# Kernel tuning notes

Hardware: AMD Instinct MI355X
Metric: run time of the kernel (lower is better)

## Reference

```python
import jax, jax.numpy as jnp
import numpy as np

DIM = 3072
DIM_HEAD = 128
HEADS = 16
KV_DIM = 2048
INNER = DIM_HEAD * HEADS  # 2048


def layernorm(x, g, b, eps=1e-5):
    mu = jnp.mean(x, axis=-1, keepdims=True)
    var = jnp.mean((x - mu) ** 2, axis=-1, keepdims=True)
    return (x - mu) * jax.lax.rsqrt(var + eps) * g + b


def setup_inputs() -> dict:
    key = jax.random.key(0)
    ks = jax.random.split(key, 6)
    b, n1, n2 = 2, 4096, 1024
    x = jax.random.normal(ks[0], (b, n1, KV_DIM), dtype=jnp.float32)
    latents = jax.random.normal(ks[1], (b, n2, DIM), dtype=jnp.float32)
    # Linear weights stored [in, out] (torch stores [out, in]; math is x @ W)
    Wq = jax.random.normal(ks[2], (DIM, INNER), dtype=jnp.float32) * 0.02
    Wkv = jax.random.normal(ks[3], (KV_DIM, 2 * INNER), dtype=jnp.float32) * 0.02
    Wout = jax.random.normal(ks[4], (INNER, DIM), dtype=jnp.float32) * 0.02
    ln1_g = jnp.ones((KV_DIM,), jnp.float32)
    ln1_b = jnp.zeros((KV_DIM,), jnp.float32)
    ln2_g = jnp.ones((DIM,), jnp.float32)
    ln2_b = jnp.zeros((DIM,), jnp.float32)
    return {"x": x, "latents": latents, "ln1_g": ln1_g, "ln1_b": ln1_b,
            "ln2_g": ln2_g, "ln2_b": ln2_b, "Wq": Wq, "Wkv": Wkv, "Wout": Wout}


def reference(x, latents, ln1_g, ln1_b, ln2_g, ln2_b, Wq, Wkv, Wout):
    b, n2, _ = latents.shape
    xn = layernorm(x, ln1_g, ln1_b)          # (b, n1, kv_dim)
    ln = layernorm(latents, ln2_g, ln2_b)    # (b, n2, dim)
    q = ln @ Wq                               # (b, n2, inner)
    kv = xn @ Wkv                             # (b, n1, 2*inner)
    k, v = jnp.split(kv, 2, axis=-1)
    # (b, seq, h*d) -> (b, h, seq, d)
    def heads(t):
        bs, L, _ = t.shape
        return t.reshape(bs, L, HEADS, DIM_HEAD).transpose(0, 2, 1, 3)
    q, k, v = heads(q), heads(k), heads(v)
    scale = 1.0 / np.sqrt(np.sqrt(DIM_HEAD)).astype(np.float32)
    logits = jnp.einsum('bhqd,bhkd->bhqk', q * scale, k * scale)
    w = jax.nn.softmax(logits.astype(jnp.float32), axis=-1).astype(logits.dtype)
    out = jnp.einsum('bhqk,bhkd->bhqd', w, v)  # (b, h, n2, d)
    out = out.transpose(0, 2, 1, 3).reshape(b, n2, INNER)
    return out @ Wout
```

## Files before the change

kernel.cpp:

```cpp
#include <hip/hip_runtime.h>
#include <stdint.h>

typedef unsigned short u16;
typedef unsigned int u32;
typedef __attribute__((ext_vector_type(4))) float f32x4;
typedef __attribute__((ext_vector_type(8))) __bf16 bf16x8;

#define N1T 4096
#define N2T 1024
#define DIMT 3072
#define KVD 2048
#define INN 2048
#define NH 16
#define DH 128

__device__ __forceinline__ u16 f2bf(float f) {
  u32 u = __builtin_bit_cast(u32, f);
  u = (u + 0x7fffu + ((u >> 16) & 1u)) >> 16;
  return (u16)u;
}

typedef __attribute__((address_space(1))) void gvoid_t;
typedef __attribute__((address_space(3))) void lvoid_t;

__device__ __forceinline__ void gload16(const void* g, void* l) {
  __builtin_amdgcn_global_load_lds((gvoid_t*)g, (lvoid_t*)l, 16, 0, 0);
}

template<int NV>
__global__ __launch_bounds__(256) void ln_cast_kernel(
    const float* __restrict__ X, const float* __restrict__ G,
    const float* __restrict__ B, u16* __restrict__ out) {
  const int D = NV * 1024;
  const int t = threadIdx.x;
  const size_t row = blockIdx.x;
  const float4* xr = (const float4*)(X + row * D);
  float4 v[NV];
  float s = 0.f, ss = 0.f;
#pragma unroll
  for (int i = 0; i < NV; ++i) {
    v[i] = xr[i * 256 + t];
    s += v[i].x + v[i].y + v[i].z + v[i].w;
    ss += v[i].x * v[i].x + v[i].y * v[i].y + v[i].z * v[i].z + v[i].w * v[i].w;
  }
#pragma unroll
  for (int off = 32; off; off >>= 1) {
    s += __shfl_xor(s, off);
    ss += __shfl_xor(ss, off);
  }
  __shared__ float red[2][4];
  const int wave = t >> 6, lane = t & 63;
  if (lane == 0) { red[0][wave] = s; red[1][wave] = ss; }
  __syncthreads();
  s = red[0][0] + red[0][1] + red[0][2] + red[0][3];
  ss = red[1][0] + red[1][1] + red[1][2] + red[1][3];
  const float mu = s / D;
  const float rstd = rsqrtf(ss / D - mu * mu + 1e-5f);
  u16* orow = out + row * D;
#pragma unroll
  for (int i = 0; i < NV; ++i) {
    const int idx = (i * 256 + t) * 4;
    float4 g4 = *(const float4*)(G + idx);
    float4 b4 = *(const float4*)(B + idx);
    union { ushort4 v4; u16 h[4]; } pk;
    pk.h[0] = f2bf((v[i].x - mu) * rstd * g4.x + b4.x);
    pk.h[1] = f2bf((v[i].y - mu) * rstd * g4.y + b4.y);
    pk.h[2] = f2bf((v[i].z - mu) * rstd * g4.z + b4.z);
    pk.h[3] = f2bf((v[i].w - mu) * rstd * g4.w + b4.w);
    *(ushort4*)(orow + idx) = pk.v4;
  }
}

__global__ __launch_bounds__(256) void tcast_kernel(
    const float* __restrict__ W, u16* __restrict__ WT, int K, int N) {
  __shared__ __align__(16) u16 tile[64][72];
  const int t = threadIdx.x;
  const int k0 = blockIdx.x * 64, n0 = blockIdx.y * 64;
#pragma unroll
  for (int i = 0; i < 4; ++i) {
    int idx = i * 256 + t;
    int r = idx >> 4, c = (idx & 15) << 2;
    float4 v = *(const float4*)(W + (size_t)(k0 + r) * N + n0 + c);
    union { ushort4 v4; u16 h[4]; } pk;
    pk.h[0] = f2bf(v.x); pk.h[1] = f2bf(v.y);
    pk.h[2] = f2bf(v.z); pk.h[3] = f2bf(v.w);
    *(ushort4*)&tile[r][c] = pk.v4;
  }
  __syncthreads();
#pragma unroll
  for (int j = 0; j < 2; ++j) {
    int cid = j * 256 + t;
    int nr = cid >> 3, kc = (cid & 7) << 3;
    union { uint4 v4; u16 h[8]; } pk;
#pragma unroll
    for (int jj = 0; jj < 8; ++jj) pk.h[jj] = tile[kc + jj][nr];
    *(uint4*)(WT + (size_t)(n0 + nr) * K + k0 + kc) = pk.v4;
  }
}

template<int BF16OUT>
__global__ __launch_bounds__(256) void gemm_bt_kernel(
    const u16* __restrict__ A, size_t Az,
    const u16* __restrict__ Bt, size_t Btz,
    void* __restrict__ Cv, size_t Cz,
    int M, int N, int K, float scale) {
  __shared__ __align__(16) u16 As[128 * 64];
  __shared__ __align__(16) u16 Bs[128 * 64];
  A += (size_t)blockIdx.z * Az;
  Bt += (size_t)blockIdx.z * Btz;
  const int t = threadIdx.x, lane = t & 63, wave = t >> 6;
  const int m0 = blockIdx.x * 128, n0 = blockIdx.y * 128;
  const int wr = (wave >> 1) * 64, wc = (wave & 1) * 64;
  const int fr = lane & 15, fk = (lane >> 4) * 8;
  f32x4 acc[4][4];
#pragma unroll
  for (int i = 0; i < 4; ++i)
#pragma unroll
    for (int j = 0; j < 4; ++j)
#pragma unroll
      for (int r = 0; r < 4; ++r) acc[i][j][r] = 0.f;
  const int srow = t >> 3;
  const int scb = (t & 7) * 16;
  const int nk = K >> 6;
  for (int kt = 0; kt < nk; ++kt) {
    const char* Ab = (const char*)(A + (size_t)kt * 64);
    const char* Bb = (const char*)(Bt + (size_t)kt * 64);
#pragma unroll
    for (int r = 0; r < 4; ++r) {
      int row = srow + r * 32;
      gload16(Ab + (size_t)(m0 + row) * K * 2 + scb, (char*)As + t * 16 + r * 4096);
      gload16(Bb + (size_t)(n0 + row) * K * 2 + scb, (char*)Bs + t * 16 + r * 4096);
    }
    __syncthreads();
#pragma unroll
    for (int kk = 0; kk < 2; ++kk) {
      bf16x8 af[4], bfr[4];
#pragma unroll
      for (int i = 0; i < 4; ++i)
        af[i] = *(const bf16x8*)&As[(wr + i * 16 + fr) * 64 + kk * 32 + fk];
#pragma unroll
      for (int j = 0; j < 4; ++j)
        bfr[j] = *(const bf16x8*)&Bs[(wc + j * 16 + fr) * 64 + kk * 32 + fk];
#pragma unroll
      for (int i = 0; i < 4; ++i)
#pragma unroll
        for (int j = 0; j < 4; ++j)
          acc[i][j] = __builtin_amdgcn_mfma_f32_16x16x32_bf16(af[i], bfr[j], acc[i][j], 0, 0, 0);
    }
    __syncthreads();
  }
  const int cr = (lane >> 4) * 4, cc = lane & 15;
#pragma unroll
  for (int i = 0; i < 4; ++i)
#pragma unroll
    for (int j = 0; j < 4; ++j) {
      const int row = m0 + wr + i * 16 + cr;
      const int col = n0 + wc + j * 16 + cc;
      if (BF16OUT) {
        u16* C = (u16*)Cv + (size_t)blockIdx.z * Cz;
#pragma unroll
        for (int r = 0; r < 4; ++r) C[(size_t)(row + r) * N + col] = f2bf(acc[i][j][r] * scale);
      } else {
        float* C = (float*)Cv + (size_t)blockIdx.z * Cz;
#pragma unroll
        for (int r = 0; r < 4; ++r) C[(size_t)(row + r) * N + col] = acc[i][j][r];
      }
    }
}

__device__ __forceinline__ void stage_region(const u16* __restrict__ G, int ldk,
                                             int rowbase, int colbase,
                                             u16* lds, int t) {
  const int srow = t >> 2, sc = t & 3;
  const int swz = (srow >> 1) & 3;
#pragma unroll
  for (int r = 0; r < 2; ++r) {
    int row = r * 128 + srow;
    gload16(G + (size_t)(rowbase + row) * ldk + colbase + (sc ^ swz) * 8,
            (char*)lds + t * 16 + r * 8192);
  }
}

#define GPHASE(MSUB, KK, STAGE_STMT, RELOAD_B, VM0)                               \
  {                                                                               \
    STAGE_STMT;                                                                   \
    const u16* Aarr = (KK) ? A1s : A0s;                                           \
    _Pragma("unroll")                                                             \
    for (int fi = 0; fi < 4; ++fi) {                                              \
      int rowa = RM + (MSUB) * 64 + fi * 16 + fr;                                 \
      af[fi] = *(const bf16x8*)((const char*)Aarr + rowa * 64 +                   \
                                ((q ^ ((rowa >> 1) & 3)) * 16));                  \
    }                                                                             \
    if (RELOAD_B) {                                                               \
      const u16* Barr = (KK) ? B1s : B0s;                                         \
      _Pragma("unroll")                                                           \
      for (int j = 0; j < 4; ++j) {                                               \
        int rowb = RN + j * 16 + fr;                                              \
        bf[j] = *(const bf16x8*)((const char*)Barr + rowb * 64 +                  \
                                 ((q ^ ((rowb >> 1) & 3)) * 16));                 \
      }                                                                           \
    }                                                                             \
    if (VM0) { asm volatile("s_waitcnt vmcnt(0)" ::: "memory"); }                 \
    else     { asm volatile("s_waitcnt vmcnt(2)" ::: "memory"); }                 \
    __builtin_amdgcn_s_barrier();                                                 \
    asm volatile("s_waitcnt lgkmcnt(0)" ::: "memory");                            \
    __builtin_amdgcn_sched_barrier(0);                                            \
    __builtin_amdgcn_s_setprio(1);                                                \
    _Pragma("unroll")                                                             \
    for (int fi = 0; fi < 4; ++fi)                                                \
      _Pragma("unroll")                                                           \
      for (int j = 0; j < 4; ++j)                                                 \
        acc[(MSUB) * 4 + fi][j] = __builtin_amdgcn_mfma_f32_16x16x32_bf16(        \
            af[fi], bf[j], acc[(MSUB) * 4 + fi][j], 0, 0, 0);                     \
    __builtin_amdgcn_s_setprio(0);                                                \
    __builtin_amdgcn_s_barrier();                                                 \
  }

template<int BF16OUT>
__global__ __launch_bounds__(512) void gemm256_kernel(
    const u16* __restrict__ A, size_t Az,
    const u16* __restrict__ Bt, size_t Btz,
    void* __restrict__ Cv, size_t Cz,
    int M, int N, int K, float scale) {
  __shared__ __align__(16) u16 A0s[256 * 32];
  __shared__ __align__(16) u16 A1s[256 * 32];
  __shared__ __align__(16) u16 B0s[256 * 32];
  __shared__ __align__(16) u16 B1s[256 * 32];
  A += (size_t)blockIdx.z * Az;
  Bt += (size_t)blockIdx.z * Btz;
  const int t = threadIdx.x, lane = t & 63, wave = t >> 6;
  const int m0 = blockIdx.x * 256, n0 = blockIdx.y * 256;
  const int RM = (wave >> 2) * 128, RN = (wave & 3) * 64;
  const int fr = lane & 15, q = lane >> 4;
  f32x4 acc[8][4];
#pragma unroll
  for (int i = 0; i < 8; ++i)
#pragma unroll
    for (int j = 0; j < 4; ++j)
#pragma unroll
      for (int r = 0; r < 4; ++r) acc[i][j][r] = 0.f;

  stage_region(Bt, K, n0, 0, B0s, t);
  stage_region(A, K, m0, 0, A0s, t);
  stage_region(Bt, K, n0, 32, B1s, t);
  asm volatile("s_waitcnt vmcnt(0)" ::: "memory");
  __builtin_amdgcn_s_barrier();

  const int nk = K >> 6;
#pragma unroll 1
  for (int kt = 0; kt < nk; ++kt) {
    const bool last = (kt == nk - 1);
    bf16x8 af[4], bf[4];
    GPHASE(0, 0, stage_region(A, K, m0, kt * 64 + 32, A1s, t), true, false)
    GPHASE(1, 0, if (!last) stage_region(Bt, K, n0, (kt + 1) * 64, B0s, t), false, last)
    GPHASE(1, 1, if (!last) stage_region(A, K, m0, (kt + 1) * 64, A0s, t), true, last)
    GPHASE(0, 1, if (!last) stage_region(Bt, K, n0, (kt + 1) * 64 + 32, B1s, t), false, last)
  }

  const int cr = (lane >> 4) * 4, cc = lane & 15;
#pragma unroll
  for (int i = 0; i < 8; ++i)
#pragma unroll
    for (int j = 0; j < 4; ++j) {
      const int row = m0 + RM + i * 16 + cr;
      const int col = n0 + RN + j * 16 + cc;
      if (BF16OUT) {
        u16* C = (u16*)Cv + (size_t)blockIdx.z * Cz;
#pragma unroll
        for (int r = 0; r < 4; ++r) C[(size_t)(row + r) * N + col] = f2bf(acc[i][j][r] * scale);
      } else {
        float* C = (float*)Cv + (size_t)blockIdx.z * Cz;
#pragma unroll
        for (int r = 0; r < 4; ++r) C[(size_t)(row + r) * N + col] = acc[i][j][r];
      }
    }
}

__device__ __forceinline__ void stage_kv(const u16* Kbase, const u16* Vbase,
                                         int kv0, char* ks, char* vs, int t) {
  const int ks_row = t >> 4, ks_cb = (t & 15) * 16;
  const int vs_row = t >> 3, vs_cb = (t & 7) * 16;
#pragma unroll
  for (int r = 0; r < 2; ++r) {
    int row = ks_row + r * 32;
    int srccb = ks_cb ^ ((row & 15) << 4);
    gload16((const char*)(Kbase + (size_t)(kv0 + row) * INN) + srccb, ks + t * 16 + r * 8192);
  }
#pragma unroll
  for (int r = 0; r < 2; ++r) {
    int row = vs_row + r * 64;
    int srccb = vs_cb ^ ((row & 7) << 4);
    gload16((const char*)(Vbase + (size_t)row * N1T + kv0) + srccb, vs + t * 16 + r * 8192);
  }
}

__global__ __launch_bounds__(512) void attn_kernel(
    const u16* __restrict__ Q, const u16* __restrict__ Kb,
    const u16* __restrict__ Vt, u16* __restrict__ O) {
  __shared__ __align__(16) u16 Ks[2][64 * 128];
  __shared__ __align__(16) u16 Vs[2][128 * 64];
  __shared__ __align__(16) u16 Ps[8][16][72];
  const int t = threadIdx.x, lane = t & 63, wave = t >> 6;
  const int bid = blockIdx.x;
  const int xcd = bid & 7, idx = bid >> 3;
  const int bh = (xcd << 2) | (idx >> 3);
  const int q0 = (idx & 7) * 128;
  const int b = bh >> 4, h = bh & 15;
  const int fr = lane & 15, fk = (lane >> 4) * 8;
  const int quad16 = (lane >> 4) * 16;

  bf16x8 qf[4];
  {
    const u16* qrow = Q + (size_t)(b * N2T + q0 + wave * 16 + fr) * INN + h * DH;
#pragma unroll
    for (int c = 0; c < 4; ++c) qf[c] = *(const bf16x8*)(qrow + c * 32 + fk);
  }
  bf16x8 ones;
#pragma unroll
  for (int j = 0; j < 8; ++j) ones[j] = (__bf16)1.0f;

  float m_run[4], l_run[4];
  f32x4 o_acc[8];
#pragma unroll
  for (int r = 0; r < 4; ++r) { m_run[r] = -1e30f; l_run[r] = 0.f; }
#pragma unroll
  for (int i = 0; i < 8; ++i)
#pragma unroll
    for (int r = 0; r < 4; ++r) o_acc[i][r] = 0.f;

  const u16* Kbase = Kb + (size_t)(b * N1T) * INN + h * DH;
  const u16* Vbase = Vt + ((size_t)b * INN + h * DH) * N1T;

  const int NT = N1T / 64;
  int cur = 0;
  stage_kv(Kbase, Vbase, 0, (char*)&Ks[0][0], (char*)&Vs[0][0], t);
  for (int tile = 0; tile < NT; ++tile) {
    if (tile + 1 < NT) {
      stage_kv(Kbase, Vbase, (tile + 1) * 64, (char*)&Ks[cur ^ 1][0],
               (char*)&Vs[cur ^ 1][0], t);
      asm volatile("s_waitcnt vmcnt(4)" ::: "memory");
    } else {
      asm volatile("s_waitcnt vmcnt(0)" ::: "memory");
    }
    __builtin_amdgcn_s_barrier();
    __builtin_amdgcn_sched_barrier(0);
    const char* KsC = (const char*)&Ks[cur][0];
    const char* VsC = (const char*)&Vs[cur][0];

    f32x4 s[4];
#pragma unroll
    for (int ni = 0; ni < 4; ++ni) {
#pragma unroll
      for (int r = 0; r < 4; ++r) s[ni][r] = 0.f;
#pragma unroll
      for (int c = 0; c < 4; ++c) {
        int row = ni * 16 + fr;
        int byteoff = row * 256 + ((c * 64 + quad16) ^ ((row & 15) << 4));
        bf16x8 kf = *(const bf16x8*)(KsC + byteoff);
        s[ni] = __builtin_amdgcn_mfma_f32_16x16x32_bf16(qf[c], kf, s[ni], 0, 0, 0);
      }
    }
    float pmax[4];
#pragma unroll
    for (int r = 0; r < 4; ++r) {
      float mt = fmaxf(fmaxf(s[0][r], s[1][r]), fmaxf(s[2][r], s[3][r]));
#pragma unroll
      for (int d = 1; d < 16; d <<= 1) mt = fmaxf(mt, __shfl_xor(mt, d));
      pmax[r] = mt;
    }
    bool ok = (pmax[0] <= m_run[0] + 8.f) & (pmax[1] <= m_run[1] + 8.f) &
              (pmax[2] <= m_run[2] + 8.f) & (pmax[3] <= m_run[3] + 8.f);
    if (!__all(ok)) {
#pragma unroll
      for (int r = 0; r < 4; ++r) {
        float mnew = fmaxf(m_run[r], pmax[r]);
        float alpha = __expf(m_run[r] - mnew);
        m_run[r] = mnew;
        l_run[r] *= alpha;
#pragma unroll
        for (int ni2 = 0; ni2 < 8; ++ni2) o_acc[ni2][r] *= alpha;
      }
    }
#pragma unroll
    for (int r = 0; r < 4; ++r)
#pragma unroll
      for (int ni = 0; ni < 4; ++ni) s[ni][r] = __expf(s[ni][r] - m_run[r]);
#pragma unroll
    for (int ni = 0; ni < 4; ++ni)
#pragma unroll
      for (int r = 0; r < 4; ++r)
        Ps[wave][(lane >> 4) * 4 + r][fr + ni * 16] = f2bf(s[ni][r]);
    asm volatile("s_waitcnt lgkmcnt(0)" ::: "memory");
    __builtin_amdgcn_sched_barrier(0);
    bf16x8 pa[2];
#pragma unroll
    for (int c2 = 0; c2 < 2; ++c2) pa[c2] = *(const bf16x8*)&Ps[wave][fr][c2 * 32 + fk];
    f32x4 lt;
#pragma unroll
    for (int r = 0; r < 4; ++r) lt[r] = 0.f;
    lt = __builtin_amdgcn_mfma_f32_16x16x32_bf16(pa[0], ones, lt, 0, 0, 0);
    lt = __builtin_amdgcn_mfma_f32_16x16x32_bf16(pa[1], ones, lt, 0, 0, 0);
#pragma unroll
    for (int r = 0; r < 4; ++r) l_run[r] += lt[r];
#pragma unroll
    for (int ni2 = 0; ni2 < 8; ++ni2) {
#pragma unroll
      for (int c2 = 0; c2 < 2; ++c2) {
        int row = ni2 * 16 + fr;
        int byteoff = row * 128 + ((c2 * 64 + quad16) ^ ((row & 7) << 4));
        bf16x8 vf = *(const bf16x8*)(VsC + byteoff);
        o_acc[ni2] = __builtin_amdgcn_mfma_f32_16x16x32_bf16(pa[c2], vf, o_acc[ni2], 0, 0, 0);
      }
    }
    __builtin_amdgcn_sched_barrier(0);
    __builtin_amdgcn_s_barrier();
    cur ^= 1;
  }
  const int cr = (lane >> 4) * 4;
  u16* orow = O + (size_t)(b * N2T + q0 + wave * 16) * INN + h * DH;
#pragma unroll
  for (int r = 0; r < 4; ++r) {
    float inv = 1.0f / l_run[r];
#pragma unroll
    for (int ni2 = 0; ni2 < 8; ++ni2)
      orow[(size_t)(cr + r) * INN + ni2 * 16 + fr] = f2bf(o_acc[ni2][r] * inv);
  }
}

extern "C" void kernel_launch(void* const* d_in, const int* in_sizes, int n_in,
                              void* d_out, int out_size, void* d_ws, size_t ws_size,
                              hipStream_t stream) {
  const float* x = (const float*)d_in[0];
  const float* latents = (const float*)d_in[1];
  const float* ln1g = (const float*)d_in[2];
  const float* ln1b = (const float*)d_in[3];
  const float* ln2g = (const float*)d_in[4];
  const float* ln2b = (const float*)d_in[5];
  const float* Wq = (const float*)d_in[6];
  const float* Wkv = (const float*)d_in[7];
  const float* Wout = (const float*)d_in[8];

  char* w = (char*)d_ws;
  u16* xn = (u16*)w;   w += (size_t)8192 * 2048 * 2;
  u16* lnb = (u16*)w;  w += (size_t)2048 * 3072 * 2;
  u16* WqT = (u16*)w;  w += (size_t)2048 * 3072 * 2;
  u16* WkvT = (u16*)w; w += (size_t)4096 * 2048 * 2;
  u16* WoT = (u16*)w;  w += (size_t)3072 * 2048 * 2;
  u16* qb = (u16*)w;   w += (size_t)2048 * 2048 * 2;
  u16* kb = (u16*)w;   w += (size_t)8192 * 2048 * 2;
  u16* vtb = (u16*)w;  w += (size_t)2 * 2048 * 4096 * 2;
  u16* ab = (u16*)w;   w += (size_t)2048 * 2048 * 2;

  dim3 blk(256);
  tcast_kernel<<<dim3(48, 32), blk, 0, stream>>>(Wq, WqT, 3072, 2048);
  tcast_kernel<<<dim3(32, 64), blk, 0, stream>>>(Wkv, WkvT, 2048, 4096);
  tcast_kernel<<<dim3(32, 48), blk, 0, stream>>>(Wout, WoT, 2048, 3072);
  ln_cast_kernel<2><<<8192, blk, 0, stream>>>(x, ln1g, ln1b, xn);
  ln_cast_kernel<3><<<2048, blk, 0, stream>>>(latents, ln2g, ln2b, lnb);

  const float scale = 0.29730177875068026f;
  gemm_bt_kernel<1><<<dim3(16, 16, 1), blk, 0, stream>>>(
      lnb, 0, WqT, 0, qb, 0, 2048, 2048, 3072, scale);
  gemm256_kernel<1><<<dim3(32, 8, 1), dim3(512), 0, stream>>>(
      xn, 0, WkvT, 0, kb, 0, 8192, 2048, 2048, scale);
  gemm256_kernel<1><<<dim3(8, 16, 2), dim3(512), 0, stream>>>(
      WkvT + (size_t)2048 * 2048, 0, xn, (size_t)4096 * 2048,
      vtb, (size_t)2048 * 4096, 2048, 4096, 2048, 1.0f);
  attn_kernel<<<dim3(256), dim3(512), 0, stream>>>(qb, kb, vtb, ab);
  gemm_bt_kernel<0><<<dim3(16, 24, 1), blk, 0, stream>>>(
      ab, 0, WoT, 0, d_out, 0, 2048, 3072, 2048, 1.0f);
}
```

Baseline: 445.7 us.

## Transpose attention MFMA to keep P in registers and double KV tile

Reworks the flash-attention inner loop so that S^T = K·Q^T is computed, with keys along rows. Each lane then holds the probabilities for one query column and can pack them straight into bf16 MFMA operands with v_cvt_pk_bf16_f32. This removes the LDS round-trip for P, the ones-matrix MFMA used for row sums, and the per-row shuffle reductions. The KV tile grows from 64 to 128 keys with a new swizzle, halving the barrier count per sequence at the cost of more LDS. Outputs are written as 4-wide vector stores, and a key permutation (frp) keeps K and P orderings consistent.

```diff
diff --git a/kernel.cpp b/kernel.cpp
--- a/kernel.cpp
+++ b/kernel.cpp
@@ -18,6 +18,12 @@
   u32 u = __builtin_bit_cast(u32, f);
   u = (u + 0x7fffu + ((u >> 16) & 1u)) >> 16;
   return (u16)u;
+}
+
+__device__ __forceinline__ u32 cvtpk(float lo, float hi) {
+  u32 r;
+  asm volatile("v_cvt_pk_bf16_f32 %0, %1, %2" : "=v"(r) : "v"(lo), "v"(hi));
+  return r;
 }
 
 typedef __attribute__((address_space(1))) void gvoid_t;
@@ -276,38 +282,42 @@
     }
 }
 
+#define KVB 128
+__device__ __forceinline__ int swz4(int row) {
+  return ((row & 15) ^ (((row >> 4) & 1) << 2)) << 4;
+}
+
 __device__ __forceinline__ void stage_kv(const u16* Kbase, const u16* Vbase,
                                          int kv0, char* ks, char* vs, int t) {
-  const int ks_row = t >> 4, ks_cb = (t & 15) * 16;
-  const int vs_row = t >> 3, vs_cb = (t & 7) * 16;
-#pragma unroll
-  for (int r = 0; r < 2; ++r) {
-    int row = ks_row + r * 32;
-    int srccb = ks_cb ^ ((row & 15) << 4);
-    gload16((const char*)(Kbase + (size_t)(kv0 + row) * INN) + srccb, ks + t * 16 + r * 8192);
-  }
-#pragma unroll
-  for (int r = 0; r < 2; ++r) {
-    int row = vs_row + r * 64;
-    int srccb = vs_cb ^ ((row & 7) << 4);
-    gload16((const char*)(Vbase + (size_t)row * N1T + kv0) + srccb, vs + t * 16 + r * 8192);
+  const int col = (t & 15) * 16;
+#pragma unroll
+  for (int r = 0; r < 4; ++r) {
+    int row = (t >> 4) + r * 32;
+    gload16((const char*)(Kbase + (size_t)(kv0 + row) * INN) + (col ^ swz4(row)),
+            ks + t * 16 + r * 8192);
+  }
+#pragma unroll
+  for (int r = 0; r < 4; ++r) {
+    int row = (t >> 4) + r * 32;
+    gload16((const char*)(Vbase + (size_t)row * N1T + kv0) + (col ^ swz4(row)),
+            vs + t * 16 + r * 8192);
   }
 }
 
 __global__ __launch_bounds__(512) void attn_kernel(
     const u16* __restrict__ Q, const u16* __restrict__ Kb,
     const u16* __restrict__ Vt, u16* __restrict__ O) {
-  __shared__ __align__(16) u16 Ks[2][64 * 128];
-  __shared__ __align__(16) u16 Vs[2][128 * 64];
-  __shared__ __align__(16) u16 Ps[8][16][72];
+  __shared__ __align__(16) u16 Ks[2][KVB * 128];
+  __shared__ __align__(16) u16 Vs[2][128 * KVB];
   const int t = threadIdx.x, lane = t & 63, wave = t >> 6;
   const int bid = blockIdx.x;
   const int xcd = bid & 7, idx = bid >> 3;
   const int bh = (xcd << 2) | (idx >> 3);
   const int q0 = (idx & 7) * 128;
   const int b = bh >> 4, h = bh & 15;
-  const int fr = lane & 15, fk = (lane >> 4) * 8;
-  const int quad16 = (lane >> 4) * 16;
+  const int fr = lane & 15, quad = lane >> 4;
+  const int fk = quad * 8;
+  const int frp = fr + (fr & 12);
 
   bf16x8 qf[4];
   {
@@ -315,30 +325,25 @@
 #pragma unroll
     for (int c = 0; c < 4; ++c) qf[c] = *(const bf16x8*)(qrow + c * 32 + fk);
   }
-  bf16x8 ones;
-#pragma unroll
-  for (int j = 0; j < 8; ++j) ones[j] = (__bf16)1.0f;
-
-  float m_run[4], l_run[4];
-  f32x4 o_acc[8];
-#pragma unroll
-  for (int r = 0; r < 4; ++r) { m_run[r] = -1e30f; l_run[r] = 0.f; }
+
+  float m_run = -1e30f, l_run = 0.f;
+  f32x4 oT[8];
 #pragma unroll
   for (int i = 0; i < 8; ++i)
 #pragma unroll
-    for (int r = 0; r < 4; ++r) o_acc[i][r] = 0.f;
+    for (int r = 0; r < 4; ++r) oT[i][r] = 0.f;
 
   const u16* Kbase = Kb + (size_t)(b * N1T) * INN + h * DH;
   const u16* Vbase = Vt + ((size_t)b * INN + h * DH) * N1T;
 
-  const int NT = N1T / 64;
+  const int NT = N1T / KVB;
   int cur = 0;
   stage_kv(Kbase, Vbase, 0, (char*)&Ks[0][0], (char*)&Vs[0][0], t);
   for (int tile = 0; tile < NT; ++tile) {
     if (tile + 1 < NT) {
-      stage_kv(Kbase, Vbase, (tile + 1) * 64, (char*)&Ks[cur ^ 1][0],
+      stage_kv(Kbase, Vbase, (tile + 1) * KVB, (char*)&Ks[cur ^ 1][0],
                (char*)&Vs[cur ^ 1][0], t);
-      asm volatile("s_waitcnt vmcnt(4)" ::: "memory");
+      asm volatile("s_waitcnt vmcnt(8)" ::: "memory");
     } else {
       asm volatile("s_waitcnt vmcnt(0)" ::: "memory");
     }
@@ -347,83 +352,77 @@
     const char* KsC = (const char*)&Ks[cur][0];
     const char* VsC = (const char*)&Vs[cur][0];
 
-    f32x4 s[4];
-#pragma unroll
-    for (int ni = 0; ni < 4; ++ni) {
-#pragma unroll
-      for (int r = 0; r < 4; ++r) s[ni][r] = 0.f;
+    f32x4 sT[8];
+#pragma unroll
+    for (int ni = 0; ni < 8; ++ni) {
+#pragma unroll
+      for (int r = 0; r < 4; ++r) sT[ni][r] = 0.f;
+      const int rowa = (ni >> 1) * 32 + (ni & 1) * 4 + frp;
+      const int sz = swz4(rowa);
 #pragma unroll
       for (int c = 0; c < 4; ++c) {
-        int row = ni * 16 + fr;
-        int byteoff = row * 256 + ((c * 64 + quad16) ^ ((row & 15) << 4));
-        bf16x8 kf = *(const bf16x8*)(KsC + byteoff);
-        s[ni] = __builtin_amdgcn_mfma_f32_16x16x32_bf16(qf[c], kf, s[ni], 0, 0, 0);
+        bf16x8 kf = *(const bf16x8*)(KsC + rowa * 256 + ((c * 64 + quad * 16) ^ sz));
+        sT[ni] = __builtin_amdgcn_mfma_f32_16x16x32_bf16(kf, qf[c], sT[ni], 0, 0, 0);
       }
     }
-    float pmax[4];
-#pragma unroll
-    for (int r = 0; r < 4; ++r) {
-      float mt = fmaxf(fmaxf(s[0][r], s[1][r]), fmaxf(s[2][r], s[3][r]));
-#pragma unroll
-      for (int d = 1; d < 16; d <<= 1) mt = fmaxf(mt, __shfl_xor(mt, d));
-      pmax[r] = mt;
-    }
-    bool ok = (pmax[0] <= m_run[0] + 8.f) & (pmax[1] <= m_run[1] + 8.f) &
-              (pmax[2] <= m_run[2] + 8.f) & (pmax[3] <= m_run[3] + 8.f);
-    if (!__all(ok)) {
+    float mt = sT[0][0];
+#pragma unroll
+    for (int ni = 0; ni < 8; ++ni)
+#pragma unroll
+      for (int r = 0; r < 4; ++r) mt = fmaxf(mt, sT[ni][r]);
+    mt = fmaxf(mt, __shfl_xor(mt, 16));
+    mt = fmaxf(mt, __shfl_xor(mt, 32));
+    if (!__all(mt <= m_run + 8.f)) {
+      float mnew = fmaxf(m_run, mt);
+      float alpha = __expf(m_run - mnew);
+      m_run = mnew;
+      l_run *= alpha;
+#pragma unroll
+      for (int i = 0; i < 8; ++i)
+#pragma unroll
+        for (int r = 0; r < 4; ++r) oT[i][r] *= alpha;
+    }
+    float lt = 0.f;
+#pragma unroll
+    for (int ni = 0; ni < 8; ++ni)
 #pragma unroll
       for (int r = 0; r < 4; ++r) {
-        float mnew = fmaxf(m_run[r], pmax[r]);
-        float alpha = __expf(m_run[r] - mnew);
-        m_run[r] = mnew;
-        l_run[r] *= alpha;
-#pragma unroll
-        for (int ni2 = 0; ni2 < 8; ++ni2) o_acc[ni2][r] *= alpha;
+        sT[ni][r] = __expf(sT[ni][r] - m_run);
+        lt += sT[ni][r];
       }
-    }
-#pragma unroll
-    for (int r = 0; r < 4; ++r)
-#pragma unroll
-      for (int ni = 0; ni < 4; ++ni) s[ni][r] = __expf(s[ni][r] - m_run[r]);
-#pragma unroll
-    for (int ni = 0; ni < 4; ++ni)
-#pragma unroll
-      for (int r = 0; r < 4; ++r)
-        Ps[wave][(lane >> 4) * 4 + r][fr + ni * 16] = f2bf(s[ni][r]);
-    asm volatile("s_waitcnt lgkmcnt(0)" ::: "memory");
-    __builtin_amdgcn_sched_barrier(0);
-    bf16x8 pa[2];
-#pragma unroll
-    for (int c2 = 0; c2 < 2; ++c2) pa[c2] = *(const bf16x8*)&Ps[wave][fr][c2 * 32 + fk];
-    f32x4 lt;
-#pragma unroll
-    for (int r = 0; r < 4; ++r) lt[r] = 0.f;
-    lt = __builtin_amdgcn_mfma_f32_16x16x32_bf16(pa[0], ones, lt, 0, 0, 0);
-    lt = __builtin_amdgcn_mfma_f32_16x16x32_bf16(pa[1], ones, lt, 0, 0, 0);
-#pragma unroll
-    for (int r = 0; r < 4; ++r) l_run[r] += lt[r];
+    lt += __shfl_xor(lt, 16);
+    lt += __shfl_xor(lt, 32);
+    l_run += lt;
+    union { u32 w[4]; bf16x8 v; } pa[4];
+#pragma unroll
+    for (int kk = 0; kk < 4; ++kk) {
+      pa[kk].w[0] = cvtpk(sT[kk * 2][0], sT[kk * 2][1]);
+      pa[kk].w[1] = cvtpk(sT[kk * 2][2], sT[kk * 2][3]);
+      pa[kk].w[2] = cvtpk(sT[kk * 2 + 1][0], sT[kk * 2 + 1][1]);
+      pa[kk].w[3] = cvtpk(sT[kk * 2 + 1][2], sT[kk * 2 + 1][3]);
+    }
 #pragma unroll
     for (int ni2 = 0; ni2 < 8; ++ni2) {
-#pragma unroll
-      for (int c2 = 0; c2 < 2; ++c2) {
-        int row = ni2 * 16 + fr;
-        int byteoff = row * 128 + ((c2 * 64 + quad16) ^ ((row & 7) << 4));
-        bf16x8 vf = *(const bf16x8*)(VsC + byteoff);
-        o_acc[ni2] = __builtin_amdgcn_mfma_f32_16x16x32_bf16(pa[c2], vf, o_acc[ni2], 0, 0, 0);
+      const int rowv = ni2 * 16 + fr;
+      const int sz = swz4(rowv);
+#pragma unroll
+      for (int kk = 0; kk < 4; ++kk) {
+        bf16x8 vf = *(const bf16x8*)(VsC + rowv * 256 + ((kk * 64 + quad * 16) ^ sz));
+        oT[ni2] = __builtin_amdgcn_mfma_f32_16x16x32_bf16(vf, pa[kk].v, oT[ni2], 0, 0, 0);
       }
     }
     __builtin_amdgcn_sched_barrier(0);
     __builtin_amdgcn_s_barrier();
     cur ^= 1;
   }
-  const int cr = (lane >> 4) * 4;
-  u16* orow = O + (size_t)(b * N2T + q0 + wave * 16) * INN + h * DH;
-#pragma unroll
-  for (int r = 0; r < 4; ++r) {
-    float inv = 1.0f / l_run[r];
-#pragma unroll
-    for (int ni2 = 0; ni2 < 8; ++ni2)
-      orow[(size_t)(cr + r) * INN + ni2 * 16 + fr] = f2bf(o_acc[ni2][r] * inv);
+  const float inv = 1.0f / l_run;
+  u16* orow = O + (size_t)(b * N2T + q0 + wave * 16 + fr) * INN + h * DH;
+#pragma unroll
+  for (int ni2 = 0; ni2 < 8; ++ni2) {
+    union { ushort4 v4; u16 hh[4]; } pk;
+#pragma unroll
+    for (int r = 0; r < 4; ++r) pk.hh[r] = f2bf(oT[ni2][r] * inv);
+    *(ushort4*)(orow + ni2 * 16 + quad * 4) = pk.v4;
   }
 }
 
```

After: 402.8 us. 9.6% less time.
